# Kernel tuning notes

Hardware: AMD Instinct MI355X
Metric: run time of the kernel (lower is better)

## Reference

```python
import jax, jax.numpy as jnp
import numpy as np

NUM_HEADS = 32
NUM_KV_HEADS = 8
HEAD_DIM = 128
HIDDEN = 4096
BASE = 10000.0


def setup_inputs() -> dict:
    key = jax.random.key(0)
    ks = jax.random.split(key, 9)
    bs, seq = 1, 2048
    x = jax.random.normal(ks[0], (bs, seq, HIDDEN), dtype=jnp.float32)
    position_ids = jnp.broadcast_to(jnp.arange(seq, dtype=jnp.int32), (bs, seq))
    s = 1.0 / np.sqrt(HIDDEN)
    wq = jax.random.normal(ks[1], (NUM_HEADS * HEAD_DIM, HIDDEN), dtype=jnp.float32) * s
    bq = jnp.zeros((NUM_HEADS * HEAD_DIM,), dtype=jnp.float32)
    wk = jax.random.normal(ks[2], (NUM_KV_HEADS * HEAD_DIM, HIDDEN), dtype=jnp.float32) * s
    bk = jnp.zeros((NUM_KV_HEADS * HEAD_DIM,), dtype=jnp.float32)
    wv = jax.random.normal(ks[3], (NUM_KV_HEADS * HEAD_DIM, HIDDEN), dtype=jnp.float32) * s
    bv = jnp.zeros((NUM_KV_HEADS * HEAD_DIM,), dtype=jnp.float32)
    wo = jax.random.normal(ks[4], (HIDDEN, NUM_HEADS * HEAD_DIM), dtype=jnp.float32) * s
    bo = jnp.zeros((HIDDEN,), dtype=jnp.float32)
    return {"x": x, "position_ids": position_ids, "wq": wq, "bq": bq,
            "wk": wk, "bk": bk, "wv": wv, "bv": bv, "wo": wo, "bo": bo}


def _rotate_half(t):
    h = t.shape[-1] // 2
    return jnp.concatenate([-t[..., h:], t[..., :h]], axis=-1)


def _rope_cos_sin(position_ids, dtype):
    # inv_freq: (head_dim/2,)
    inv_freq = 1.0 / (BASE ** (jnp.arange(0, HEAD_DIM, 2, dtype=jnp.float32) / HEAD_DIM))
    freqs = position_ids.astype(jnp.float32)[..., None] * inv_freq  # (bs, seq, hd/2)
    emb = jnp.concatenate([freqs, freqs], axis=-1)  # (bs, seq, hd)
    return jnp.cos(emb).astype(dtype), jnp.sin(emb).astype(dtype)


def reference(x, position_ids, wq, bq, wk, bk, wv, bv, wo, bo):
    bs, seq, _ = x.shape
    g = NUM_HEADS // NUM_KV_HEADS
    # projections -> (bs, heads, seq, head_dim)
    q = (x @ wq.T + bq).reshape(bs, seq, NUM_HEADS, HEAD_DIM).transpose(0, 2, 1, 3)
    k = (x @ wk.T + bk).reshape(bs, seq, NUM_KV_HEADS, HEAD_DIM).transpose(0, 2, 1, 3)
    v = (x @ wv.T + bv).reshape(bs, seq, NUM_KV_HEADS, HEAD_DIM).transpose(0, 2, 1, 3)
    cos, sin = _rope_cos_sin(position_ids, x.dtype)
    cos, sin = cos[:, None], sin[:, None]  # broadcast over heads
    q = q * cos + _rotate_half(q) * sin
    k = k * cos + _rotate_half(k) * sin
    # grouped attention without expanding kv (same math as repeat_kv)
    qg = q.reshape(bs, NUM_KV_HEADS, g, seq, HEAD_DIM)
    scores = jnp.einsum('bhgqd,bhkd->bhgqk', qg, k) / jnp.sqrt(
        jnp.asarray(HEAD_DIM, dtype=jnp.float32)).astype(x.dtype)
    probs = jax.nn.softmax(scores.astype(jnp.float32), axis=-1).astype(x.dtype)
    out = jnp.einsum('bhgqk,bhkd->bhgqd', probs, v)  # (bs, kvh, g, seq, hd)
    out = out.reshape(bs, NUM_HEADS, seq, HEAD_DIM).transpose(0, 2, 1, 3)
    out = out.reshape(bs, seq, NUM_HEADS * HEAD_DIM)
    return out @ wo.T + bo
```

## Files before the change

kernel.cpp:

```cpp
#include <hip/hip_runtime.h>
#include <stdint.h>

typedef unsigned short u16;
typedef unsigned long long u64;
typedef __attribute__((ext_vector_type(8))) short s8v;
typedef __attribute__((ext_vector_type(4))) float f4v;

#define MFMA(a, b, c) __builtin_amdgcn_mfma_f32_16x16x32_bf16((a), (b), (c), 0, 0, 0)

__device__ __forceinline__ u16 f2b(float f) {
  uint32_t x = __float_as_uint(f);
  x += 0x7fff + ((x >> 16) & 1);
  return (u16)(x >> 16);
}
__device__ __forceinline__ float b2f(u16 u) {
  return __uint_as_float(((uint32_t)u) << 16);
}

__device__ __forceinline__ void gll16(const void* g, void* l) {
  __builtin_amdgcn_global_load_lds((const __attribute__((address_space(1))) uint32_t*)g,
                                   (__attribute__((address_space(3))) uint32_t*)l, 16, 0, 0);
}
__device__ __forceinline__ void bar() { __builtin_amdgcn_s_barrier(); }

__global__ void cvt_all(const float* __restrict__ x, const float* __restrict__ wq,
                        const float* __restrict__ wk, const float* __restrict__ wv,
                        const float* __restrict__ wo,
                        u16* __restrict__ xb, u16* __restrict__ wqkv, u16* __restrict__ wob) {
  int i = blockIdx.x * 256 + threadIdx.x;
  const float* s; u16* d; size_t off;
  if      (i < 1048576) { s = x;  d = xb;   off = (size_t)i; }
  else if (i < 3145728) { s = wq; d = wqkv; off = (size_t)(i - 1048576); }
  else if (i < 3670016) { s = wk; d = wqkv + (size_t)16777216; off = (size_t)(i - 3145728); }
  else if (i < 4194304) { s = wv; d = wqkv + (size_t)20971520; off = (size_t)(i - 3670016); }
  else                  { s = wo; d = wob;  off = (size_t)(i - 4194304); }
  const float4* sp = (const float4*)(s + off * 8);
  float4 f0 = sp[0], f1 = sp[1];
  s8v o;
  o[0] = (short)f2b(f0.x); o[1] = (short)f2b(f0.y); o[2] = (short)f2b(f0.z); o[3] = (short)f2b(f0.w);
  o[4] = (short)f2b(f1.x); o[5] = (short)f2b(f1.y); o[6] = (short)f2b(f1.z); o[7] = (short)f2b(f1.w);
  *(s8v*)(d + off * 8) = o;
}

template <int BM, int MODE>
__global__ __launch_bounds__(256, 2) void gemm2p(
    const u16* __restrict__ A, const u16* __restrict__ Bact,
    const float* __restrict__ bias,
    float* __restrict__ Cf, u16* __restrict__ Cq, u16* __restrict__ Ck, u16* __restrict__ Cv,
    int K) {
  extern __shared__ u16 smem[];
  constexpr int AO = BM * 64;
  constexpr int BE = 2 * BM * 64;
  constexpr int MI = BM / 32;
  constexpr int AR = BM / 16;

  const int tid = threadIdx.x;
  const int l = tid & 63, wv = tid >> 6;
  const int lr = l & 15, lg = l >> 4;
  const int swz = 16 * (lr & 7);

  const int nwg = gridDim.x;
  int bid = blockIdx.x;
  bid = (bid & 7) * (nwg >> 3) + (bid >> 3);
  const int NB = 8;
  const int m0 = (bid / NB) * BM, n0 = (bid % NB) * 256;

  const int sr = tid >> 3;
  const int sc = ((tid & 7) ^ (sr & 7)) * 8;
  const u16* gA = A + (size_t)(m0 + sr) * K + sc;
  const u16* gB = Bact + (size_t)(n0 + sr) * K + sc;

  auto STA = [&](int P, int h, int kt) {
    gll16(gA + (size_t)(h * 32) * K + (size_t)kt * 64,
          smem + (P ? AO : 0) + h * 2048 + tid * 8);
  };
  auto STB = [&](int kt) {
#pragma unroll
    for (int rr = 0; rr < 8; ++rr)
      gll16(gB + (size_t)(rr * 32) * K + (size_t)kt * 64,
            smem + BE + rr * 2048 + tid * 8);
  };

  const char* smc = (const char*)smem;
  s8v a[MI][2], b0[2][2], b1[2][2];
  auto LDA = [&](int P, int QR) {
#pragma unroll
    for (int mi = 0; mi < MI; ++mi)
#pragma unroll
      for (int kk = 0; kk < 2; ++kk)
        a[mi][kk] = *(const s8v*)(smc + (P ? AO * 2 : 0) +
            (QR * (BM / 2) + mi * 16 + lr) * 128 + ((kk * 64 + lg * 16) ^ swz));
  };
  auto LDB = [&](int QC, s8v bb[2][2]) {
#pragma unroll
    for (int ni = 0; ni < 2; ++ni)
#pragma unroll
      for (int kk = 0; kk < 2; ++kk)
        bb[ni][kk] = *(const s8v*)(smc + BE * 2 +
            (wv * 64 + QC * 32 + ni * 16 + lr) * 128 + ((kk * 64 + lg * 16) ^ swz));
  };

  f4v acc[AR][4];
#pragma unroll
  for (int i = 0; i < AR; ++i)
#pragma unroll
    for (int j = 0; j < 4; ++j) acc[i][j] = {0.f, 0.f, 0.f, 0.f};

#define PHMF(QR, QC, B)                                                        \
  __builtin_amdgcn_s_setprio(1);                                               \
  _Pragma("unroll") for (int mi = 0; mi < MI; ++mi)                            \
    _Pragma("unroll") for (int ni = 0; ni < 2; ++ni)                           \
      _Pragma("unroll") for (int kk = 0; kk < 2; ++kk)                         \
        acc[(QR) * MI + mi][(QC) * 2 + ni] =                                   \
            MFMA(a[mi][kk], B[ni][kk], acc[(QR) * MI + mi][(QC) * 2 + ni]);    \
  __builtin_amdgcn_s_setprio(0);

#pragma unroll
  for (int h = 0; h < MI; ++h) STA(0, h, 0);
  STB(0);
  asm volatile("s_waitcnt vmcnt(0)" ::: "memory");
  bar();

  const int ITERS = K >> 6;
  for (int i = 0; i < ITERS; ++i) {
    const int P = i & 1;
    const bool more = (i + 1 < ITERS);
    LDA(P, 0); LDB(0, b0); LDB(1, b1);
    if (more) {
#pragma unroll
      for (int h = 0; h < MI; ++h) STA(P ^ 1, h, i + 1);
    }
    bar();
    PHMF(0, 0, b0); PHMF(0, 1, b1);
    bar();
    LDA(P, 1);
    if (more) STB(i + 1);
    bar();
    PHMF(1, 1, b1); PHMF(1, 0, b0);
    asm volatile("s_waitcnt vmcnt(0)" ::: "memory");
    bar();
  }
#undef PHMF

  bar();

  if constexpr (MODE == 2) {
#pragma unroll
    for (int ai = 0; ai < AR; ++ai) {
      const int f0 = m0 + ai * 16;
      if (f0 >= 5120) {
#pragma unroll
        for (int fj = 0; fj < 4; ++fj)
#pragma unroll
          for (int r = 0; r < 4; ++r) {
            const int f = f0 + lg * 4 + r;
            const int tok = n0 + wv * 64 + fj * 16 + lr;
            Cv[(size_t)(f - 5120) * 2048 + tok] = f2b(acc[ai][fj][r] + bias[f]);
          }
      }
    }
    if (m0 < 5120) {
      u16* buf = smem + wv * 3328;
#pragma unroll
      for (int c = 0; c < 2; ++c) {
#pragma unroll
        for (int fj2 = 0; fj2 < 2; ++fj2) {
          const int fj = 2 * c + fj2;
          const int tl = fj2 * 16 + lr;
#pragma unroll
          for (int ai = 0; ai < AR; ++ai) {
            const int f0 = m0 + ai * 16;
            if (f0 < 5120) {
#pragma unroll
              for (int r = 0; r < 4; ++r) {
                const int fl = ai * 16 + lg * 4 + r;
                buf[tl * 104 + fl] = f2b(acc[ai][fj][r] + bias[m0 + fl]);
              }
            }
          }
        }
        asm volatile("s_waitcnt lgkmcnt(0)" ::: "memory");
        const int row = l >> 1, half = l & 1;
        const int tok = n0 + wv * 64 + c * 32 + row;
#pragma unroll
        for (int i2 = 0; i2 < AR; ++i2) {
          const int flc = (2 * i2 + half) * 8;
          const int f = m0 + flc;
          if (f < 4096)
            *(s8v*)(Cq + (size_t)tok * 4096 + f) = *(const s8v*)(buf + row * 104 + flc);
          else if (f < 5120)
            *(s8v*)(Ck + (size_t)tok * 1024 + (f - 4096)) = *(const s8v*)(buf + row * 104 + flc);
        }
        asm volatile("s_waitcnt lgkmcnt(0)" ::: "memory");
      }
    }
  } else {
    float* buf = (float*)smem + wv * 1088;
#pragma unroll
    for (int c = 0; c < 4; ++c) {
#pragma unroll
      for (int ai = 0; ai < AR; ++ai)
#pragma unroll
        for (int r = 0; r < 4; ++r) {
          const int fl = ai * 16 + lg * 4 + r;
          buf[lr * 68 + fl] = acc[ai][c][r] + bias[m0 + fl];
        }
      asm volatile("s_waitcnt lgkmcnt(0)" ::: "memory");
      const int row = l >> 2, q4 = l & 3;
      const int tok = n0 + wv * 64 + c * 16 + row;
      float* g = Cf + (size_t)tok * 4096 + m0 + q4 * 16;
      const float* src = buf + row * 68 + q4 * 16;
#pragma unroll
      for (int i2 = 0; i2 < 4; ++i2)
        *(f4v*)(g + i2 * 4) = *(const f4v*)(src + i2 * 4);
      asm volatile("s_waitcnt lgkmcnt(0)" ::: "memory");
    }
  }
}

__global__ void rope_kernel(u16* __restrict__ q, u16* __restrict__ k, const int* __restrict__ pos) {
  int i = blockIdx.x * 256 + threadIdx.x;
  const int NQ = 2048 * 32 * 64;
  const int NK = 2048 * 8 * 64;
  u16* buf;
  int m, d, stride, h;
  if (i < NQ) { buf = q; m = i >> 11; h = (i >> 6) & 31; d = i & 63; stride = 4096; }
  else {
    i -= NQ; if (i >= NK) return;
    buf = k; m = i >> 9; h = (i >> 6) & 7; d = i & 63; stride = 1024;
  }
  size_t base = (size_t)m * stride + h * 128 + d;
  float a = b2f(buf[base]), b = b2f(buf[base + 64]);
  float p = (float)pos[m];
  float ang = p * exp2f(-0.20762050593045952f * (float)d);
  float s, c;
  sincosf(ang, &s, &c);
  buf[base]      = f2b(a * c - b * s);
  buf[base + 64] = f2b(b * c + a * s);
}

__global__ __launch_bounds__(256, 2) void attn_kernel(const u16* __restrict__ Q, const u16* __restrict__ Kb,
                                                      const u16* __restrict__ Vt, u16* __restrict__ Ao) {
  __shared__ __align__(16) u16 Ks[64 * 128];
  __shared__ __align__(16) u16 Vs[128 * 64];
  __shared__ __align__(16) u16 Ps[4][32 * 64];
  const int tid = threadIdx.x;
  const int l = tid & 63, wv = tid >> 6;
  const int lr = l & 15, lg = l >> 4;
  const int head = blockIdx.x >> 4, qt = blockIdx.x & 15;
  const int kh = head >> 2;
  const int qrow = qt * 128 + wv * 32 + lr;

  s8v qf[2][4];
#pragma unroll
  for (int qh = 0; qh < 2; ++qh)
#pragma unroll
    for (int s = 0; s < 4; ++s)
      qf[qh][s] = *(const s8v*)&Q[(size_t)(qrow + qh * 16) * 4096 + head * 128 + s * 32 + lg * 8];

  f4v zero = {0.f, 0.f, 0.f, 0.f};
  f4v ao[2][8];
#pragma unroll
  for (int qh = 0; qh < 2; ++qh)
#pragma unroll
    for (int tt = 0; tt < 8; ++tt) ao[qh][tt] = zero;
  float mrun[2] = {-1e30f, -1e30f}, lrun[2] = {0.f, 0.f};

  const u16* Kg = Kb + kh * 128;
  const u16* Vg = Vt + (size_t)(kh * 128) * 2048;
  const u16* kp[4];
  const u16* vp[4];
#pragma unroll
  for (int p = 0; p < 4; ++p) {
    const int ki = tid + 256 * p;
    const int kr = ki >> 4, kc = (ki & 15) ^ (kr & 7);
    kp[p] = Kg + (size_t)kr * 1024 + kc * 8;
    const int vr = ki >> 3, vc = (ki & 7) ^ (vr & 7);
    vp[p] = Vg + (size_t)vr * 2048 + vc * 8;
  }

  char* KsB = (char*)Ks;
  char* VsB = (char*)Vs;
  char* PwB = (char*)Ps[wv];
  const int swz = 16 * (lr & 7);
  const float C2 = 0.12753102f;

  for (int t = 0; t < 2048; t += 64) {
    __syncthreads();
#pragma unroll
    for (int p = 0; p < 4; ++p) {
      gll16(kp[p] + (size_t)t * 1024, KsB + (tid + 256 * p) * 16);
      gll16(vp[p] + t,                VsB + (tid + 256 * p) * 16);
    }
    __syncthreads();

    f4v c[2][4];
#pragma unroll
    for (int qh = 0; qh < 2; ++qh)
#pragma unroll
      for (int j = 0; j < 4; ++j) c[qh][j] = zero;
#pragma unroll
    for (int s = 0; s < 4; ++s) {
#pragma unroll
      for (int j = 0; j < 4; ++j) {
        s8v kf = *(const s8v*)(KsB + (16 * j + lr) * 256 + (((4 * s + lg) * 16) ^ swz));
        c[0][j] = MFMA(kf, qf[0][s], c[0][j]);
        c[1][j] = MFMA(kf, qf[1][s], c[1][j]);
      }
    }

#pragma unroll
    for (int qh = 0; qh < 2; ++qh) {
      float mx = fmaxf(fmaxf(c[qh][0][0], c[qh][0][1]), fmaxf(c[qh][0][2], c[qh][0][3]));
#pragma unroll
      for (int j = 1; j < 4; ++j)
        mx = fmaxf(mx, fmaxf(fmaxf(c[qh][j][0], c[qh][j][1]), fmaxf(c[qh][j][2], c[qh][j][3])));
      mx = fmaxf(mx, __shfl_xor(mx, 16));
      mx = fmaxf(mx, __shfl_xor(mx, 32));
      float m2x = mx * C2;

      if (!__all(m2x - mrun[qh] <= 8.f)) {
        float mnew = fmaxf(mrun[qh], m2x);
        float alpha = __builtin_amdgcn_exp2f(mrun[qh] - mnew);
        float ar[4];
#pragma unroll
        for (int r = 0; r < 4; ++r) ar[r] = __shfl(alpha, 4 * lg + r);
#pragma unroll
        for (int tt = 0; tt < 8; ++tt)
#pragma unroll
          for (int r = 0; r < 4; ++r) ao[qh][tt][r] *= ar[r];
        lrun[qh] *= alpha;
        mrun[qh] = mnew;
      }

      float rs = 0.f;
#pragma unroll
      for (int j = 0; j < 4; ++j) {
        float p0 = __builtin_amdgcn_exp2f(__builtin_fmaf(c[qh][j][0], C2, -mrun[qh]));
        float p1 = __builtin_amdgcn_exp2f(__builtin_fmaf(c[qh][j][1], C2, -mrun[qh]));
        float p2 = __builtin_amdgcn_exp2f(__builtin_fmaf(c[qh][j][2], C2, -mrun[qh]));
        float p3 = __builtin_amdgcn_exp2f(__builtin_fmaf(c[qh][j][3], C2, -mrun[qh]));
        rs += (p0 + p1) + (p2 + p3);
        uint32_t lo = (uint32_t)f2b(p0) | ((uint32_t)f2b(p1) << 16);
        uint32_t hi = (uint32_t)f2b(p2) | ((uint32_t)f2b(p3) << 16);
        u64 pak = (u64)lo | ((u64)hi << 32);
        *(u64*)(PwB + (qh * 16 + lr) * 128 + ((32 * j + 8 * lg) ^ swz)) = pak;
      }
      rs += __shfl_xor(rs, 16);
      rs += __shfl_xor(rs, 32);
      lrun[qh] += rs;
    }

#pragma unroll
    for (int h = 0; h < 2; ++h) {
      s8v pf0 = *(const s8v*)(PwB + lr * 128 + ((64 * h + 16 * lg) ^ swz));
      s8v pf1 = *(const s8v*)(PwB + (16 + lr) * 128 + ((64 * h + 16 * lg) ^ swz));
#pragma unroll
      for (int tt = 0; tt < 8; ++tt) {
        s8v vf = *(const s8v*)(VsB + (16 * tt + lr) * 128 + (((4 * h + lg) * 16) ^ swz));
        ao[0][tt] = MFMA(pf0, vf, ao[0][tt]);
        ao[1][tt] = MFMA(pf1, vf, ao[1][tt]);
      }
    }
  }

#pragma unroll
  for (int qh = 0; qh < 2; ++qh) {
    float inv = 1.f / lrun[qh];
    float ir[4];
#pragma unroll
    for (int r = 0; r < 4; ++r) ir[r] = __shfl(inv, 4 * lg + r);
#pragma unroll
    for (int tt = 0; tt < 8; ++tt)
#pragma unroll
      for (int r = 0; r < 4; ++r)
        Ao[(size_t)(qt * 128 + wv * 32 + qh * 16 + 4 * lg + r) * 4096 + head * 128 + 16 * tt + lr] =
            f2b(ao[qh][tt][r] * ir[r]);
  }
}

extern "C" void kernel_launch(void* const* d_in, const int* in_sizes, int n_in,
                              void* d_out, int out_size, void* d_ws, size_t ws_size,
                              hipStream_t stream) {
  const float* x  = (const float*)d_in[0];
  const int*   pos = (const int*)d_in[1];
  const float* wq = (const float*)d_in[2];
  const float* bq = (const float*)d_in[3];
  const float* wk = (const float*)d_in[4];
  const float* bk = (const float*)d_in[5];
  const float* wv = (const float*)d_in[6];
  const float* bv = (const float*)d_in[7];
  const float* wo = (const float*)d_in[8];
  const float* bo = (const float*)d_in[9];
  float* out = (float*)d_out;

  char* ws = (char*)d_ws;
  u16* xb   = (u16*)(ws + 0);
  u16* wqkv = (u16*)(ws + 16777216);
  u16* wob  = (u16*)(ws + 67108864);
  u16* qb   = (u16*)(ws + 100663296);
  u16* kb   = (u16*)(ws + 117440512);
  u16* vT   = (u16*)(ws + 121634816);
  u16* ab   = (u16*)(ws + 125829120);
  float* bqkv = (float*)(ws + 142606336);

  hipMemcpyAsync(bqkv,        bq, 4096 * sizeof(float), hipMemcpyDeviceToDevice, stream);
  hipMemcpyAsync(bqkv + 4096, bk, 1024 * sizeof(float), hipMemcpyDeviceToDevice, stream);
  hipMemcpyAsync(bqkv + 5120, bv, 1024 * sizeof(float), hipMemcpyDeviceToDevice, stream);

  cvt_all<<<24576, 256, 0, stream>>>(x, wq, wk, wv, wo, xb, wqkv, wob);

  gemm2p<96, 2><<<512, 256, 57344, stream>>>(wqkv, xb, bqkv,
                                             nullptr, qb, kb, vT, 4096);
  rope_kernel<<<(2048 * 32 * 64 + 2048 * 8 * 64) / 256, 256, 0, stream>>>(qb, kb, pos);
  attn_kernel<<<512, 256, 0, stream>>>(qb, kb, vT, ab);
  gemm2p<64, 0><<<512, 256, 49152, stream>>>(wob, ab, bo,
                                             out, nullptr, nullptr, nullptr, 4096);
}
```

Baseline: 328.5 us.

## Double-buffer K/V tiles and split attention across 8 waves of 16 rows

The attention kernel moves to 512 threads, with each of 8 waves owning 16 query rows instead of 4 waves owning 32. K/V tiles are now double-buffered in LDS, so the next tile's global-to-LDS load is issued before computing on the current one, with one barrier per iteration instead of two. The aim is to hide load latency and cut per-wave register pressure for more latency tolerance. In exchange, each K/V fragment read from LDS feeds half as many MFMAs, so LDS traffic per FLOP rises, and LDS use grows to about 80KB per block.

```diff
diff --git a/kernel.cpp b/kernel.cpp
--- a/kernel.cpp
+++ b/kernel.cpp
@@ -239,144 +239,135 @@
   buf[base + 64] = f2b(b * c + a * s);
 }
 
-__global__ __launch_bounds__(256, 2) void attn_kernel(const u16* __restrict__ Q, const u16* __restrict__ Kb,
+__global__ __launch_bounds__(512, 4) void attn_kernel(const u16* __restrict__ Q, const u16* __restrict__ Kb,
                                                       const u16* __restrict__ Vt, u16* __restrict__ Ao) {
-  __shared__ __align__(16) u16 Ks[64 * 128];
-  __shared__ __align__(16) u16 Vs[128 * 64];
-  __shared__ __align__(16) u16 Ps[4][32 * 64];
+  __shared__ __align__(16) u16 Ks[2][64 * 128];
+  __shared__ __align__(16) u16 Vs[2][128 * 64];
+  __shared__ __align__(16) u16 Ps[8][16 * 64];
   const int tid = threadIdx.x;
   const int l = tid & 63, wv = tid >> 6;
   const int lr = l & 15, lg = l >> 4;
   const int head = blockIdx.x >> 4, qt = blockIdx.x & 15;
   const int kh = head >> 2;
-  const int qrow = qt * 128 + wv * 32 + lr;
-
-  s8v qf[2][4];
-#pragma unroll
-  for (int qh = 0; qh < 2; ++qh)
-#pragma unroll
-    for (int s = 0; s < 4; ++s)
-      qf[qh][s] = *(const s8v*)&Q[(size_t)(qrow + qh * 16) * 4096 + head * 128 + s * 32 + lg * 8];
+  const int qrow = qt * 128 + wv * 16 + lr;
+
+  s8v qf[4];
+#pragma unroll
+  for (int s = 0; s < 4; ++s)
+    qf[s] = *(const s8v*)&Q[(size_t)qrow * 4096 + head * 128 + s * 32 + lg * 8];
 
   f4v zero = {0.f, 0.f, 0.f, 0.f};
-  f4v ao[2][8];
-#pragma unroll
-  for (int qh = 0; qh < 2; ++qh)
-#pragma unroll
-    for (int tt = 0; tt < 8; ++tt) ao[qh][tt] = zero;
-  float mrun[2] = {-1e30f, -1e30f}, lrun[2] = {0.f, 0.f};
-
+  f4v ao[8];
+#pragma unroll
+  for (int tt = 0; tt < 8; ++tt) ao[tt] = zero;
+  float mrun = -1e30f, lrun = 0.f;
+
+  const int ki0 = tid, ki1 = tid + 512;
+  const int kr0 = ki0 >> 4, kc0 = (ki0 & 15) ^ (kr0 & 7);
+  const int kr1 = ki1 >> 4, kc1 = (ki1 & 15) ^ (kr1 & 7);
+  const int vr0 = ki0 >> 3, vc0 = (ki0 & 7) ^ (vr0 & 7);
+  const int vr1 = ki1 >> 3, vc1 = (ki1 & 7) ^ (vr1 & 7);
   const u16* Kg = Kb + kh * 128;
   const u16* Vg = Vt + (size_t)(kh * 128) * 2048;
-  const u16* kp[4];
-  const u16* vp[4];
-#pragma unroll
-  for (int p = 0; p < 4; ++p) {
-    const int ki = tid + 256 * p;
-    const int kr = ki >> 4, kc = (ki & 15) ^ (kr & 7);
-    kp[p] = Kg + (size_t)kr * 1024 + kc * 8;
-    const int vr = ki >> 3, vc = (ki & 7) ^ (vr & 7);
-    vp[p] = Vg + (size_t)vr * 2048 + vc * 8;
-  }
-
-  char* KsB = (char*)Ks;
-  char* VsB = (char*)Vs;
+  const u16* kp0 = Kg + (size_t)kr0 * 1024 + kc0 * 8;
+  const u16* kp1 = Kg + (size_t)kr1 * 1024 + kc1 * 8;
+  const u16* vp0 = Vg + (size_t)vr0 * 2048 + vc0 * 8;
+  const u16* vp1 = Vg + (size_t)vr1 * 2048 + vc1 * 8;
+
+  auto stage = [&](int b, int t) {
+    gll16(kp0 + (size_t)t * 1024, (char*)Ks[b] + ki0 * 16);
+    gll16(kp1 + (size_t)t * 1024, (char*)Ks[b] + ki1 * 16);
+    gll16(vp0 + t,                (char*)Vs[b] + ki0 * 16);
+    gll16(vp1 + t,                (char*)Vs[b] + ki1 * 16);
+  };
+
   char* PwB = (char*)Ps[wv];
   const int swz = 16 * (lr & 7);
   const float C2 = 0.12753102f;
 
+  stage(0, 0);
+  __syncthreads();
+
   for (int t = 0; t < 2048; t += 64) {
-    __syncthreads();
-#pragma unroll
-    for (int p = 0; p < 4; ++p) {
-      gll16(kp[p] + (size_t)t * 1024, KsB + (tid + 256 * p) * 16);
-      gll16(vp[p] + t,                VsB + (tid + 256 * p) * 16);
-    }
-    __syncthreads();
-
-    f4v c[2][4];
-#pragma unroll
-    for (int qh = 0; qh < 2; ++qh)
-#pragma unroll
-      for (int j = 0; j < 4; ++j) c[qh][j] = zero;
+    const int cur = (t >> 6) & 1;
+    if (t + 64 < 2048) stage(cur ^ 1, t + 64);
+    const char* KsB = (const char*)Ks[cur];
+    const char* VsB = (const char*)Vs[cur];
+
+    f4v c[4];
+#pragma unroll
+    for (int j = 0; j < 4; ++j) c[j] = zero;
 #pragma unroll
     for (int s = 0; s < 4; ++s) {
 #pragma unroll
       for (int j = 0; j < 4; ++j) {
         s8v kf = *(const s8v*)(KsB + (16 * j + lr) * 256 + (((4 * s + lg) * 16) ^ swz));
-        c[0][j] = MFMA(kf, qf[0][s], c[0][j]);
-        c[1][j] = MFMA(kf, qf[1][s], c[1][j]);
+        c[j] = MFMA(kf, qf[s], c[j]);
       }
     }
 
-#pragma unroll
-    for (int qh = 0; qh < 2; ++qh) {
-      float mx = fmaxf(fmaxf(c[qh][0][0], c[qh][0][1]), fmaxf(c[qh][0][2], c[qh][0][3]));
-#pragma unroll
-      for (int j = 1; j < 4; ++j)
-        mx = fmaxf(mx, fmaxf(fmaxf(c[qh][j][0], c[qh][j][1]), fmaxf(c[qh][j][2], c[qh][j][3])));
-      mx = fmaxf(mx, __shfl_xor(mx, 16));
-      mx = fmaxf(mx, __shfl_xor(mx, 32));
-      float m2x = mx * C2;
-
-      if (!__all(m2x - mrun[qh] <= 8.f)) {
-        float mnew = fmaxf(mrun[qh], m2x);
-        float alpha = __builtin_amdgcn_exp2f(mrun[qh] - mnew);
-        float ar[4];
-#pragma unroll
-        for (int r = 0; r < 4; ++r) ar[r] = __shfl(alpha, 4 * lg + r);
-#pragma unroll
-        for (int tt = 0; tt < 8; ++tt)
-#pragma unroll
-          for (int r = 0; r < 4; ++r) ao[qh][tt][r] *= ar[r];
-        lrun[qh] *= alpha;
-        mrun[qh] = mnew;
-      }
-
-      float rs = 0.f;
-#pragma unroll
-      for (int j = 0; j < 4; ++j) {
-        float p0 = __builtin_amdgcn_exp2f(__builtin_fmaf(c[qh][j][0], C2, -mrun[qh]));
-        float p1 = __builtin_amdgcn_exp2f(__builtin_fmaf(c[qh][j][1], C2, -mrun[qh]));
-        float p2 = __builtin_amdgcn_exp2f(__builtin_fmaf(c[qh][j][2], C2, -mrun[qh]));
-        float p3 = __builtin_amdgcn_exp2f(__builtin_fmaf(c[qh][j][3], C2, -mrun[qh]));
-        rs += (p0 + p1) + (p2 + p3);
-        uint32_t lo = (uint32_t)f2b(p0) | ((uint32_t)f2b(p1) << 16);
-        uint32_t hi = (uint32_t)f2b(p2) | ((uint32_t)f2b(p3) << 16);
-        u64 pak = (u64)lo | ((u64)hi << 32);
-        *(u64*)(PwB + (qh * 16 + lr) * 128 + ((32 * j + 8 * lg) ^ swz)) = pak;
-      }
-      rs += __shfl_xor(rs, 16);
-      rs += __shfl_xor(rs, 32);
-      lrun[qh] += rs;
-    }
+    float mx = fmaxf(fmaxf(c[0][0], c[0][1]), fmaxf(c[0][2], c[0][3]));
+#pragma unroll
+    for (int j = 1; j < 4; ++j)
+      mx = fmaxf(mx, fmaxf(fmaxf(c[j][0], c[j][1]), fmaxf(c[j][2], c[j][3])));
+    mx = fmaxf(mx, __shfl_xor(mx, 16));
+    mx = fmaxf(mx, __shfl_xor(mx, 32));
+    float m2x = mx * C2;
+
+    if (!__all(m2x - mrun <= 8.f)) {
+      float mnew = fmaxf(mrun, m2x);
+      float alpha = __builtin_amdgcn_exp2f(mrun - mnew);
+      float ar[4];
+#pragma unroll
+      for (int r = 0; r < 4; ++r) ar[r] = __shfl(alpha, 4 * lg + r);
+#pragma unroll
+      for (int tt = 0; tt < 8; ++tt)
+#pragma unroll
+        for (int r = 0; r < 4; ++r) ao[tt][r] *= ar[r];
+      lrun *= alpha;
+      mrun = mnew;
+    }
+
+    float rs = 0.f;
+#pragma unroll
+    for (int j = 0; j < 4; ++j) {
+      float p0 = __builtin_amdgcn_exp2f(__builtin_fmaf(c[j][0], C2, -mrun));
+      float p1 = __builtin_amdgcn_exp2f(__builtin_fmaf(c[j][1], C2, -mrun));
+      float p2 = __builtin_amdgcn_exp2f(__builtin_fmaf(c[j][2], C2, -mrun));
+      float p3 = __builtin_amdgcn_exp2f(__builtin_fmaf(c[j][3], C2, -mrun));
+      rs += (p0 + p1) + (p2 + p3);
+      uint32_t lo = (uint32_t)f2b(p0) | ((uint32_t)f2b(p1) << 16);
+      uint32_t hi = (uint32_t)f2b(p2) | ((uint32_t)f2b(p3) << 16);
+      u64 pak = (u64)lo | ((u64)hi << 32);
+      *(u64*)(PwB + lr * 128 + ((32 * j + 8 * lg) ^ swz)) = pak;
+    }
+    rs += __shfl_xor(rs, 16);
+    rs += __shfl_xor(rs, 32);
+    lrun += rs;
 
 #pragma unroll
     for (int h = 0; h < 2; ++h) {
-      s8v pf0 = *(const s8v*)(PwB + lr * 128 + ((64 * h + 16 * lg) ^ swz));
-      s8v pf1 = *(const s8v*)(PwB + (16 + lr) * 128 + ((64 * h + 16 * lg) ^ swz));
+      s8v pf = *(const s8v*)(PwB + lr * 128 + ((64 * h + 16 * lg) ^ swz));
 #pragma unroll
       for (int tt = 0; tt < 8; ++tt) {
         s8v vf = *(const s8v*)(VsB + (16 * tt + lr) * 128 + (((4 * h + lg) * 16) ^ swz));
-        ao[0][tt] = MFMA(pf0, vf, ao[0][tt]);
-        ao[1][tt] = MFMA(pf1, vf, ao[1][tt]);
+        ao[tt] = MFMA(pf, vf, ao[tt]);
       }
     }
+
+    __syncthreads();
   }
 
-#pragma unroll
-  for (int qh = 0; qh < 2; ++qh) {
-    float inv = 1.f / lrun[qh];
-    float ir[4];
-#pragma unroll
-    for (int r = 0; r < 4; ++r) ir[r] = __shfl(inv, 4 * lg + r);
-#pragma unroll
-    for (int tt = 0; tt < 8; ++tt)
-#pragma unroll
-      for (int r = 0; r < 4; ++r)
-        Ao[(size_t)(qt * 128 + wv * 32 + qh * 16 + 4 * lg + r) * 4096 + head * 128 + 16 * tt + lr] =
-            f2b(ao[qh][tt][r] * ir[r]);
-  }
+  float inv = 1.f / lrun;
+  float ir[4];
+#pragma unroll
+  for (int r = 0; r < 4; ++r) ir[r] = __shfl(inv, 4 * lg + r);
+#pragma unroll
+  for (int tt = 0; tt < 8; ++tt)
+#pragma unroll
+    for (int r = 0; r < 4; ++r)
+      Ao[(size_t)(qt * 128 + wv * 16 + 4 * lg + r) * 4096 + head * 128 + 16 * tt + lr] =
+          f2b(ao[tt][r] * ir[r]);
 }
 
 extern "C" void kernel_launch(void* const* d_in, const int* in_sizes, int n_in,
@@ -413,7 +404,7 @@
   gemm2p<96, 2><<<512, 256, 57344, stream>>>(wqkv, xb, bqkv,
                                              nullptr, qb, kb, vT, 4096);
   rope_kernel<<<(2048 * 32 * 64 + 2048 * 8 * 64) / 256, 256, 0, stream>>>(qb, kb, pos);
-  attn_kernel<<<512, 256, 0, stream>>>(qb, kb, vT, ab);
+  attn_kernel<<<512, 512, 0, stream>>>(qb, kb, vT, ab);
   gemm2p<64, 0><<<512, 256, 49152, stream>>>(wob, ab, bo,
                                              out, nullptr, nullptr, nullptr, 4096);
 }
```

New measurement: 330.0 us. Within noise of the previous version (+0.5%).
